# Kernel optimization log

Measured on AMD Instinct MI355X. Metric: run time of the kernel, lower is better.

Reference implementation:

```python
import jax, jax.numpy as jnp
import numpy as np

B, DIM, HEADS, H, W = 4, 64, 64, 256, 256


def _conv1x1(x, w):
    # x: [b,c,h,w], w: [o,c] -> [b,o,h,w]
    return jnp.einsum('bchw,oc->bohw', x, w)


def _conv3x3_s2_reflect(x, w, groups):
    # reflect pad 1, 3x3 conv, stride 2 (matches padding_mode='reflect', stride=2)
    xp = jnp.pad(x, ((0, 0), (0, 0), (1, 1), (1, 1)), mode='reflect')
    return jax.lax.conv_general_dilated(
        xp, w, window_strides=(2, 2), padding='VALID',
        dimension_numbers=('NCHW', 'OIHW', 'NCHW'), feature_group_count=groups)


def _to_heads(t, heads):
    # safe_rearrange: zero-pad channels to a multiple of heads, then b (head c) h w -> b head c (h w)
    b, c, h, w = t.shape
    if c % heads != 0:
        t = jnp.pad(t, ((0, 0), (0, heads - c % heads), (0, 0), (0, 0)))
        c = t.shape[1]
    return t.reshape(b, heads, c // heads, h * w)


def _l2norm(t, eps=1e-12):
    # F.normalize(dim=-1): x / max(||x||, eps)
    n = jnp.sqrt(jnp.sum(t * t, axis=-1, keepdims=True))
    return t / jnp.maximum(n, eps)


def setup_inputs() -> dict:
    key = jax.random.key(0)
    ks = jax.random.split(key, 13)
    d = DIM
    s = 0.05
    return {
        'x': jax.random.normal(ks[0], (B, d, H, W), jnp.float32),
        'illu_feat': jax.random.uniform(ks[1], (B, d, H, W), jnp.float32),
        'w_q_spec': jax.random.normal(ks[2], (d, d), jnp.float32) * s,
        'w_k_spec': jax.random.normal(ks[3], (d, d), jnp.float32) * s,
        'w_v_spec': jax.random.normal(ks[4], (d, d), jnp.float32) * s,
        'w_q_spat': jax.random.normal(ks[5], (d, 1, 3, 3), jnp.float32) * s,  # depthwise
        'w_k_spat': jax.random.normal(ks[6], (d, d, 3, 3), jnp.float32) * s,
        'w_v_spat': jax.random.normal(ks[7], (d, d), jnp.float32) * s,
        'w_anchor_dw': jax.random.normal(ks[8], (d, 1, 3, 3), jnp.float32) * s,  # depthwise
        'w_anchor_pw': jax.random.normal(ks[9], (d // 2, d), jnp.float32) * s,
        'w_proj': jax.random.normal(ks[10], (d, d), jnp.float32) * s,
        'temp_spec': jnp.ones((HEADS, 1, 1), jnp.float32),
        'temp_spat': jnp.ones((HEADS, 1, 1), jnp.float32),
    }


def reference(x, illu_feat, w_q_spec, w_k_spec, w_v_spec, w_q_spat, w_k_spat,
              w_v_spat, w_anchor_dw, w_anchor_pw, w_proj, temp_spec, temp_spat):
    b, c, h, w = x.shape
    heads = HEADS

    q_spec = _conv1x1(x, w_q_spec)
    k_spec = _conv1x1(x, w_k_spec)                       # computed but unused downstream (as in original)
    v_spec = _conv1x1(x, w_v_spec) * illu_feat
    q_spat = _conv3x3_s2_reflect(x, w_q_spat, groups=c)  # computed but unused downstream (as in original)
    k_spat = _conv3x3_s2_reflect(x, w_k_spat, groups=1)
    v_spat = _conv1x1(x, w_v_spat) * illu_feat
    anchor = _conv1x1(_conv3x3_s2_reflect(x, w_anchor_dw, groups=c), w_anchor_pw)

    q_spec = _l2norm(_to_heads(q_spec, heads))
    k_spec = _l2norm(_to_heads(k_spec, heads))
    v_spec = _to_heads(v_spec, heads)
    q_spat = _l2norm(_to_heads(q_spat, heads))
    k_spat = _to_heads(k_spat, heads)
    v_spat = _to_heads(v_spat, heads)
    anchor = _l2norm(_to_heads(anchor, heads))

    n_q = q_spec.shape[-1]      # h*w
    n_a = anchor.shape[-1]      # (h//2)*(w//2)
    n_v = v_spec.shape[-1]
    n_k = k_spat.shape[-1]

    # spectral branch: q x anchor (truncate to common spatial length)
    m = min(n_q, n_a)
    attn_spec = jnp.einsum('bhcn,bhdn->bhcd', q_spec[..., :m], anchor[..., :m]) * temp_spec
    attn_spec = jax.nn.softmax(attn_spec, axis=-1)

    # v_spec spatial matching via adaptive avg pool (static no-op here since n_v == n_q)
    if n_v != n_q:
        vh = int(n_v ** 0.5)
        qh = int(n_q ** 0.5)
        v4 = v_spec.reshape(b, heads, v_spec.shape[2], vh, vh)
        v4 = jax.image.resize(v4, (b, heads, v_spec.shape[2], qh, qh), method='linear')
        v_spec_matched = v4.reshape(b, heads, v_spec.shape[2], -1)
    else:
        v_spec_matched = v_spec

    # spatial branch: anchor x k_spat (truncate to common spatial length)
    m2 = min(n_a, n_k)
    attn_spat = jnp.einsum('bhcn,bhdn->bhcd', anchor[..., :m2], k_spat[..., :m2]) * temp_spat
    attn_spat = jax.nn.softmax(attn_spat, axis=-1)

    out_spec = jnp.einsum('bhcd,bhdn->bhcn', attn_spec, v_spec_matched)
    out_spat = jnp.einsum('bhcd,bhdn->bhcn', attn_spat, v_spat)

    m3 = min(out_spec.shape[-1], out_spat.shape[-1])
    out = 0.6 * out_spec[..., :m3] + 0.4 * out_spat[..., :m3]

    ah = int(m3 ** 0.5)
    out = out.reshape(b, heads * out.shape[2], ah, ah)
    if ah != h or ah != w:
        # F.interpolate bilinear, align_corners=False == half-pixel linear resize
        out = jax.image.resize(out, (b, out.shape[1], h, w), method='bilinear')
    out = out[:, :DIM]
    return _conv1x1(out, w_proj)
```

## Files before the change

### kernel.cpp

```cpp
#include <hip/hip_runtime.h>


#define HW 65536
#define CH 64
#define PT 64
#define SX 68

typedef short s4_t __attribute__((ext_vector_type(4)));
typedef short s8_t __attribute__((ext_vector_type(8)));
typedef float f4_t __attribute__((ext_vector_type(4)));

typedef const __attribute__((address_space(1))) unsigned int* gp_t;
typedef __attribute__((address_space(3))) unsigned int* lp_t;

static __device__ __forceinline__ unsigned short f2bf(float f) {
  unsigned u = __float_as_uint(f);
  return (unsigned short)((u + 0x7fffu + ((u >> 16) & 1u)) >> 16);
}
static __device__ __forceinline__ s8_t ld8(const unsigned short* p) {
  s4_t lo = *(const s4_t*)p;
  s4_t hi = *(const s4_t*)(p + 4);
  s8_t r = {lo[0], lo[1], lo[2], lo[3], hi[0], hi[1], hi[2], hi[3]};
  return r;
}
static __device__ __forceinline__ void gload16(const float* g, float* l) {
  __builtin_amdgcn_global_load_lds((gp_t)(unsigned long long)g,
                                   (lp_t)(unsigned long long)l, 16, 0, 0);
}

__global__ __launch_bounds__(256, 2) void fused_hsattn(
    const float* __restrict__ x, const float* __restrict__ illu,
    const float* __restrict__ wvs, const float* __restrict__ wvt,
    const float* __restrict__ wproj, float* __restrict__ out) {
  __shared__ __align__(16) float xs[CH * PT];
  __shared__ __align__(16) float ils[CH * PT];
  __shared__ __align__(16) unsigned short XH[PT * SX];
  __shared__ __align__(16) unsigned short WM[CH * SX];
  __shared__ __align__(16) unsigned short WP[CH * SX];

  const int tid  = threadIdx.x;
  const int bb   = blockIdx.x >> 10;
  const int pix0 = (blockIdx.x & 1023) << 6;
  const int base = bb * CH * HW + pix0;
  const int lane = tid & 63;
  const int wv   = tid >> 6;

  f4_t wa[4], wb[4], wc[4];
#pragma unroll
  for (int it = 0; it < 4; ++it) {
    int j4 = (it * 256 + tid) * 4;
    wa[it] = *(const f4_t*)(wvs + j4);
    wb[it] = *(const f4_t*)(wvt + j4);
    wc[it] = *(const f4_t*)(wproj + j4);
  }

#pragma unroll
  for (int it = 0; it < 4; ++it) {
    int u = wv * 1024 + it * 256;
    int f = u + lane * 4;
    int c = f >> 6, p = f & 63;
    gload16(x + base + c * HW + p, xs + u);
    gload16(illu + base + c * HW + p, ils + u);
  }

#pragma unroll
  for (int it = 0; it < 4; ++it) {
    int idx = it * 256 + tid;
    int r = idx >> 4, c4 = (idx & 15) * 4;
    s4_t m, w;
#pragma unroll
    for (int j = 0; j < 4; ++j) {
      m[j] = (short)f2bf(0.6f * wa[it][j] + 0.4f * wb[it][j]);
      w[j] = (short)f2bf(wc[it][j]);
    }
    *(s4_t*)(WM + r * SX + c4) = m;
    *(s4_t*)(WP + r * SX + c4) = w;
  }
  __syncthreads();

  {
    const int p = tid & 63, cc = (tid >> 6) << 4;
#pragma unroll
    for (int k = 0; k < 16; k += 2) {
      float f0 = xs[(cc + k) * PT + p];
      float f1 = xs[(cc + k + 1) * PT + p];
      unsigned pk = (unsigned)f2bf(f0) | ((unsigned)f2bf(f1) << 16);
      *(unsigned*)(XH + p * SX + cc + k) = pk;
    }
  }
  __syncthreads();

  const int n15 = lane & 15, q = lane >> 4;
  const int nb  = wv * 16;

  f4_t acc[4];
#pragma unroll
  for (int i = 0; i < 4; ++i) acc[i] = (f4_t){0.f, 0.f, 0.f, 0.f};
#pragma unroll
  for (int kc = 0; kc < 2; ++kc) {
    s8_t B = ld8(XH + (nb + n15) * SX + kc * 32 + q * 8);
#pragma unroll
    for (int mt = 0; mt < 4; ++mt) {
      s8_t A = ld8(WM + (mt * 16 + n15) * SX + kc * 32 + q * 8);
      acc[mt] = __builtin_amdgcn_mfma_f32_16x16x32_bf16(A, B, acc[mt], 0, 0, 0);
    }
  }

  s4_t uh[4];
#pragma unroll
  for (int mt = 0; mt < 4; ++mt) {
    s4_t h;
#pragma unroll
    for (int r = 0; r < 4; ++r) {
      int c = mt * 16 + q * 4 + r;
      h[r] = (short)f2bf(acc[mt][r] * ils[c * PT + nb + n15]);
    }
    uh[mt] = h;
  }
#pragma unroll
  for (int mt = 0; mt < 4; ++mt)
    *(s4_t*)(XH + (nb + n15) * SX + mt * 16 + q * 4) = uh[mt];

  f4_t acc2[4];
#pragma unroll
  for (int i = 0; i < 4; ++i) acc2[i] = (f4_t){0.f, 0.f, 0.f, 0.f};
#pragma unroll
  for (int kc = 0; kc < 2; ++kc) {
    s8_t B = ld8(XH + (nb + n15) * SX + kc * 32 + q * 8);
#pragma unroll
    for (int mt = 0; mt < 4; ++mt) {
      s8_t A = ld8(WP + (mt * 16 + n15) * SX + kc * 32 + q * 8);
      acc2[mt] = __builtin_amdgcn_mfma_f32_16x16x32_bf16(A, B, acc2[mt], 0, 0, 0);
    }
  }

#pragma unroll
  for (int mt = 0; mt < 4; ++mt) {
    float* op = out + base + (mt * 16 + q * 4) * HW + nb + n15;
    f4_t a = acc2[mt];
#pragma unroll
    for (int r = 0; r < 4; ++r) op[r * HW] = a[r];
  }
}

extern "C" void kernel_launch(void* const* d_in, const int* in_sizes, int n_in,
                              void* d_out, int out_size, void* d_ws, size_t ws_size,
                              hipStream_t stream) {
  const float* x     = (const float*)d_in[0];
  const float* illu  = (const float*)d_in[1];
  const float* wvs   = (const float*)d_in[4];
  const float* wvt   = (const float*)d_in[7];
  const float* wproj = (const float*)d_in[10];
  float* out = (float*)d_out;

  fused_hsattn<<<4 * (HW / PT), 256, 0, stream>>>(x, illu, wvs, wvt, wproj, out);
}
```

Measured before the change: 201.8 us.

## Load activations directly into MFMA registers and loop four tiles per block with prefetch

The kernel stops staging x and illu through LDS with global_load_lds. Each lane now loads its MFMA operand elements straight from global memory into registers. Each block processes four pixel tiles in sequence, prefetching the next tile's x and illu while computing the current one. This also spreads the per-block weight setup over more work and raises occupancy to 4 blocks per SM. In exchange the global loads become scalar and strided per lane, 4 bytes per channel row with 16 consecutive pixels, instead of 16-byte vector loads. Register pressure also rises, and there is no barrier between the XH write and read across tiles, which is only safe because each wave owns its own XH rows.

```diff
diff --git a/kernel.cpp b/kernel.cpp
--- a/kernel.cpp
+++ b/kernel.cpp
@@ -5,13 +5,11 @@
 #define CH 64
 #define PT 64
 #define SX 68
+#define TPB 4
 
 typedef short s4_t __attribute__((ext_vector_type(4)));
 typedef short s8_t __attribute__((ext_vector_type(8)));
 typedef float f4_t __attribute__((ext_vector_type(4)));
-
-typedef const __attribute__((address_space(1))) unsigned int* gp_t;
-typedef __attribute__((address_space(3))) unsigned int* lp_t;
 
 static __device__ __forceinline__ unsigned short f2bf(float f) {
   unsigned u = __float_as_uint(f);
@@ -23,27 +21,26 @@
   s8_t r = {lo[0], lo[1], lo[2], lo[3], hi[0], hi[1], hi[2], hi[3]};
   return r;
 }
-static __device__ __forceinline__ void gload16(const float* g, float* l) {
-  __builtin_amdgcn_global_load_lds((gp_t)(unsigned long long)g,
-                                   (lp_t)(unsigned long long)l, 16, 0, 0);
-}
 
-__global__ __launch_bounds__(256, 2) void fused_hsattn(
+__global__ __launch_bounds__(256, 4) void fused_hsattn(
     const float* __restrict__ x, const float* __restrict__ illu,
     const float* __restrict__ wvs, const float* __restrict__ wvt,
     const float* __restrict__ wproj, float* __restrict__ out) {
-  __shared__ __align__(16) float xs[CH * PT];
-  __shared__ __align__(16) float ils[CH * PT];
-  __shared__ __align__(16) unsigned short XH[PT * SX];
   __shared__ __align__(16) unsigned short WM[CH * SX];
   __shared__ __align__(16) unsigned short WP[CH * SX];
+  __shared__ __align__(16) unsigned short XH[PT * SX];
 
   const int tid  = threadIdx.x;
-  const int bb   = blockIdx.x >> 10;
-  const int pix0 = (blockIdx.x & 1023) << 6;
-  const int base = bb * CH * HW + pix0;
   const int lane = tid & 63;
   const int wv   = tid >> 6;
+  const int n15  = lane & 15;
+  const int q    = lane >> 4;
+  const int nb   = wv * 16;
+
+  const int tile0 = blockIdx.x * TPB;
+  const int bb    = tile0 >> 10;
+  const int pix0  = (tile0 & 1023) << 6;
+  const int base0 = bb * CH * HW + pix0;
 
   f4_t wa[4], wb[4], wc[4];
 #pragma unroll
@@ -54,13 +51,20 @@
     wc[it] = *(const f4_t*)(wproj + j4);
   }
 
+  float xv[16], iv[16];
+  {
+    const float* xb = x + base0 + nb + n15;
+    const float* ib = illu + base0 + nb + n15;
 #pragma unroll
-  for (int it = 0; it < 4; ++it) {
-    int u = wv * 1024 + it * 256;
-    int f = u + lane * 4;
-    int c = f >> 6, p = f & 63;
-    gload16(x + base + c * HW + p, xs + u);
-    gload16(illu + base + c * HW + p, ils + u);
+    for (int kc = 0; kc < 2; ++kc)
+#pragma unroll
+      for (int j = 0; j < 8; ++j)
+        xv[kc * 8 + j] = xb[(kc * 32 + q * 8 + j) * HW];
+#pragma unroll
+    for (int mt = 0; mt < 4; ++mt)
+#pragma unroll
+      for (int r = 0; r < 4; ++r)
+        iv[mt * 4 + r] = ib[(mt * 16 + q * 4 + r) * HW];
   }
 
 #pragma unroll
@@ -78,68 +82,75 @@
   }
   __syncthreads();
 
-  {
-    const int p = tid & 63, cc = (tid >> 6) << 4;
 #pragma unroll
-    for (int k = 0; k < 16; k += 2) {
-      float f0 = xs[(cc + k) * PT + p];
-      float f1 = xs[(cc + k + 1) * PT + p];
-      unsigned pk = (unsigned)f2bf(f0) | ((unsigned)f2bf(f1) << 16);
-      *(unsigned*)(XH + p * SX + cc + k) = pk;
+  for (int t = 0; t < TPB; ++t) {
+    const int base = base0 + t * PT;
+
+    s8_t B0, B1;
+#pragma unroll
+    for (int j = 0; j < 8; ++j) {
+      B0[j] = (short)f2bf(xv[j]);
+      B1[j] = (short)f2bf(xv[8 + j]);
     }
-  }
-  __syncthreads();
 
-  const int n15 = lane & 15, q = lane >> 4;
-  const int nb  = wv * 16;
+    if (t + 1 < TPB) {
+      const float* xb = x + base0 + (t + 1) * PT + nb + n15;
+#pragma unroll
+      for (int kc = 0; kc < 2; ++kc)
+#pragma unroll
+        for (int j = 0; j < 8; ++j)
+          xv[kc * 8 + j] = xb[(kc * 32 + q * 8 + j) * HW];
+    }
 
-  f4_t acc[4];
+    f4_t acc[4];
 #pragma unroll
-  for (int i = 0; i < 4; ++i) acc[i] = (f4_t){0.f, 0.f, 0.f, 0.f};
-#pragma unroll
-  for (int kc = 0; kc < 2; ++kc) {
-    s8_t B = ld8(XH + (nb + n15) * SX + kc * 32 + q * 8);
+    for (int i = 0; i < 4; ++i) acc[i] = (f4_t){0.f, 0.f, 0.f, 0.f};
 #pragma unroll
     for (int mt = 0; mt < 4; ++mt) {
-      s8_t A = ld8(WM + (mt * 16 + n15) * SX + kc * 32 + q * 8);
-      acc[mt] = __builtin_amdgcn_mfma_f32_16x16x32_bf16(A, B, acc[mt], 0, 0, 0);
+      s8_t A0 = ld8(WM + (mt * 16 + n15) * SX + q * 8);
+      acc[mt] = __builtin_amdgcn_mfma_f32_16x16x32_bf16(A0, B0, acc[mt], 0, 0, 0);
+      s8_t A1 = ld8(WM + (mt * 16 + n15) * SX + 32 + q * 8);
+      acc[mt] = __builtin_amdgcn_mfma_f32_16x16x32_bf16(A1, B1, acc[mt], 0, 0, 0);
     }
-  }
 
-  s4_t uh[4];
-#pragma unroll
-  for (int mt = 0; mt < 4; ++mt) {
-    s4_t h;
-#pragma unroll
-    for (int r = 0; r < 4; ++r) {
-      int c = mt * 16 + q * 4 + r;
-      h[r] = (short)f2bf(acc[mt][r] * ils[c * PT + nb + n15]);
-    }
-    uh[mt] = h;
-  }
-#pragma unroll
-  for (int mt = 0; mt < 4; ++mt)
-    *(s4_t*)(XH + (nb + n15) * SX + mt * 16 + q * 4) = uh[mt];
-
-  f4_t acc2[4];
-#pragma unroll
-  for (int i = 0; i < 4; ++i) acc2[i] = (f4_t){0.f, 0.f, 0.f, 0.f};
-#pragma unroll
-  for (int kc = 0; kc < 2; ++kc) {
-    s8_t B = ld8(XH + (nb + n15) * SX + kc * 32 + q * 8);
 #pragma unroll
     for (int mt = 0; mt < 4; ++mt) {
-      s8_t A = ld8(WP + (mt * 16 + n15) * SX + kc * 32 + q * 8);
-      acc2[mt] = __builtin_amdgcn_mfma_f32_16x16x32_bf16(A, B, acc2[mt], 0, 0, 0);
+      s4_t h;
+#pragma unroll
+      for (int r = 0; r < 4; ++r)
+        h[r] = (short)f2bf(acc[mt][r] * iv[mt * 4 + r]);
+      *(s4_t*)(XH + (nb + n15) * SX + mt * 16 + q * 4) = h;
     }
-  }
+
+    if (t + 1 < TPB) {
+      const float* ib = illu + base0 + (t + 1) * PT + nb + n15;
+#pragma unroll
+      for (int mt = 0; mt < 4; ++mt)
+#pragma unroll
+        for (int r = 0; r < 4; ++r)
+          iv[mt * 4 + r] = ib[(mt * 16 + q * 4 + r) * HW];
+    }
+
+    f4_t acc2[4];
+#pragma unroll
+    for (int i = 0; i < 4; ++i) acc2[i] = (f4_t){0.f, 0.f, 0.f, 0.f};
+#pragma unroll
+    for (int kc = 0; kc < 2; ++kc) {
+      s8_t B = ld8(XH + (nb + n15) * SX + kc * 32 + q * 8);
+#pragma unroll
+      for (int mt = 0; mt < 4; ++mt) {
+        s8_t A = ld8(WP + (mt * 16 + n15) * SX + kc * 32 + q * 8);
+        acc2[mt] = __builtin_amdgcn_mfma_f32_16x16x32_bf16(A, B, acc2[mt], 0, 0, 0);
+      }
+    }
 
 #pragma unroll
-  for (int mt = 0; mt < 4; ++mt) {
-    float* op = out + base + (mt * 16 + q * 4) * HW + nb + n15;
-    f4_t a = acc2[mt];
+    for (int mt = 0; mt < 4; ++mt) {
+      float* op = out + base + (mt * 16 + q * 4) * HW + nb + n15;
+      f4_t a = acc2[mt];
 #pragma unroll
-    for (int r = 0; r < 4; ++r) op[r * HW] = a[r];
+      for (int r = 0; r < 4; ++r) op[r * HW] = a[r];
+    }
   }
 }
 
@@ -153,5 +164,6 @@
   const float* wproj = (const float*)d_in[10];
   float* out = (float*)d_out;
 
-  fused_hsattn<<<4 * (HW / PT), 256, 0, stream>>>(x, illu, wvs, wvt, wproj, out);
+  fused_hsattn<<<4 * (HW / PT) / TPB, 256, 0, stream>>>(x, illu, wvs, wvt,
+                                                        wproj, out);
 }
```

After: 274.9 us. +36.3%, slower.

## Process multiple 128-pixel tiles per block with register-prefetched loads

Applied to the files above, without the earlier changes.

Each block now handles four tiles of 128 pixels instead of one 64-pixel tile. Inputs are loaded into registers and the next tile is prefetched while the current one is computed. The async global-to-LDS path and the fp32 x staging buffer are gone: x goes straight from registers into LDS as transposed bf16, and illu is stored with a padded stride. The goal is to cut the per-block cost of weight setup and launch and to overlap memory latency with MFMA work, at the cost of more registers and fewer blocks.

```diff
diff --git a/kernel.cpp b/kernel.cpp
--- a/kernel.cpp
+++ b/kernel.cpp
@@ -1,17 +1,16 @@
 #include <hip/hip_runtime.h>
 
 
-#define HW 65536
-#define CH 64
-#define PT 64
-#define SX 68
+#define HW    65536
+#define CHHW  (64 * 65536)
+#define PT    128
+#define SXT   68
+#define SIL   132
+#define TPB   4
 
 typedef short s4_t __attribute__((ext_vector_type(4)));
 typedef short s8_t __attribute__((ext_vector_type(8)));
 typedef float f4_t __attribute__((ext_vector_type(4)));
-
-typedef const __attribute__((address_space(1))) unsigned int* gp_t;
-typedef __attribute__((address_space(3))) unsigned int* lp_t;
 
 static __device__ __forceinline__ unsigned short f2bf(float f) {
   unsigned u = __float_as_uint(f);
@@ -23,27 +22,24 @@
   s8_t r = {lo[0], lo[1], lo[2], lo[3], hi[0], hi[1], hi[2], hi[3]};
   return r;
 }
-static __device__ __forceinline__ void gload16(const float* g, float* l) {
-  __builtin_amdgcn_global_load_lds((gp_t)(unsigned long long)g,
-                                   (lp_t)(unsigned long long)l, 16, 0, 0);
-}
 
 __global__ __launch_bounds__(256, 2) void fused_hsattn(
     const float* __restrict__ x, const float* __restrict__ illu,
     const float* __restrict__ wvs, const float* __restrict__ wvt,
     const float* __restrict__ wproj, float* __restrict__ out) {
-  __shared__ __align__(16) float xs[CH * PT];
-  __shared__ __align__(16) float ils[CH * PT];
-  __shared__ __align__(16) unsigned short XH[PT * SX];
-  __shared__ __align__(16) unsigned short WM[CH * SX];
-  __shared__ __align__(16) unsigned short WP[CH * SX];
+  __shared__ __align__(16) unsigned short WM[64 * SXT];
+  __shared__ __align__(16) unsigned short WP[64 * SXT];
+  __shared__ __align__(16) unsigned short XT[PT * SXT];
+  __shared__ __align__(16) float ILS[64 * SIL];
 
   const int tid  = threadIdx.x;
-  const int bb   = blockIdx.x >> 10;
-  const int pix0 = (blockIdx.x & 1023) << 6;
-  const int base = bb * CH * HW + pix0;
   const int lane = tid & 63;
   const int wv   = tid >> 6;
+  const int n15  = lane & 15;
+  const int q    = lane >> 4;
+
+  const int ch0 = wv * 16 + (lane >> 5);
+  const int pxl = (lane & 31) * 4;
 
   f4_t wa[4], wb[4], wc[4];
 #pragma unroll
@@ -54,13 +50,16 @@
     wc[it] = *(const f4_t*)(wproj + j4);
   }
 
+  f4_t xr[8], ir[8];
+  {
+    const int g    = blockIdx.x * TPB;
+    const int base = (g >> 9) * CHHW + ((g & 511) << 7);
 #pragma unroll
-  for (int it = 0; it < 4; ++it) {
-    int u = wv * 1024 + it * 256;
-    int f = u + lane * 4;
-    int c = f >> 6, p = f & 63;
-    gload16(x + base + c * HW + p, xs + u);
-    gload16(illu + base + c * HW + p, ils + u);
+    for (int it = 0; it < 8; ++it) {
+      const int off = base + (ch0 + 2 * it) * HW + pxl;
+      xr[it] = *(const f4_t*)(x + off);
+      ir[it] = *(const f4_t*)(illu + off);
+    }
   }
 
 #pragma unroll
@@ -73,73 +72,88 @@
       m[j] = (short)f2bf(0.6f * wa[it][j] + 0.4f * wb[it][j]);
       w[j] = (short)f2bf(wc[it][j]);
     }
-    *(s4_t*)(WM + r * SX + c4) = m;
-    *(s4_t*)(WP + r * SX + c4) = w;
-  }
-  __syncthreads();
-
-  {
-    const int p = tid & 63, cc = (tid >> 6) << 4;
-#pragma unroll
-    for (int k = 0; k < 16; k += 2) {
-      float f0 = xs[(cc + k) * PT + p];
-      float f1 = xs[(cc + k + 1) * PT + p];
-      unsigned pk = (unsigned)f2bf(f0) | ((unsigned)f2bf(f1) << 16);
-      *(unsigned*)(XH + p * SX + cc + k) = pk;
-    }
-  }
-  __syncthreads();
-
-  const int n15 = lane & 15, q = lane >> 4;
-  const int nb  = wv * 16;
-
-  f4_t acc[4];
-#pragma unroll
-  for (int i = 0; i < 4; ++i) acc[i] = (f4_t){0.f, 0.f, 0.f, 0.f};
-#pragma unroll
-  for (int kc = 0; kc < 2; ++kc) {
-    s8_t B = ld8(XH + (nb + n15) * SX + kc * 32 + q * 8);
-#pragma unroll
-    for (int mt = 0; mt < 4; ++mt) {
-      s8_t A = ld8(WM + (mt * 16 + n15) * SX + kc * 32 + q * 8);
-      acc[mt] = __builtin_amdgcn_mfma_f32_16x16x32_bf16(A, B, acc[mt], 0, 0, 0);
-    }
-  }
-
-  s4_t uh[4];
-#pragma unroll
-  for (int mt = 0; mt < 4; ++mt) {
-    s4_t h;
-#pragma unroll
-    for (int r = 0; r < 4; ++r) {
-      int c = mt * 16 + q * 4 + r;
-      h[r] = (short)f2bf(acc[mt][r] * ils[c * PT + nb + n15]);
-    }
-    uh[mt] = h;
-  }
-#pragma unroll
-  for (int mt = 0; mt < 4; ++mt)
-    *(s4_t*)(XH + (nb + n15) * SX + mt * 16 + q * 4) = uh[mt];
-
-  f4_t acc2[4];
-#pragma unroll
-  for (int i = 0; i < 4; ++i) acc2[i] = (f4_t){0.f, 0.f, 0.f, 0.f};
-#pragma unroll
-  for (int kc = 0; kc < 2; ++kc) {
-    s8_t B = ld8(XH + (nb + n15) * SX + kc * 32 + q * 8);
-#pragma unroll
-    for (int mt = 0; mt < 4; ++mt) {
-      s8_t A = ld8(WP + (mt * 16 + n15) * SX + kc * 32 + q * 8);
-      acc2[mt] = __builtin_amdgcn_mfma_f32_16x16x32_bf16(A, B, acc2[mt], 0, 0, 0);
-    }
+    *(s4_t*)(WM + r * SXT + c4) = m;
+    *(s4_t*)(WP + r * SXT + c4) = w;
   }
 
 #pragma unroll
-  for (int mt = 0; mt < 4; ++mt) {
-    float* op = out + base + (mt * 16 + q * 4) * HW + nb + n15;
-    f4_t a = acc2[mt];
+  for (int t = 0; t < TPB; ++t) {
+    const int g    = blockIdx.x * TPB + t;
+    const int base = (g >> 9) * CHHW + ((g & 511) << 7);
+
 #pragma unroll
-    for (int r = 0; r < 4; ++r) op[r * HW] = a[r];
+    for (int it = 0; it < 8; ++it) {
+      const int ch = ch0 + 2 * it;
+      f4_t v = xr[it];
+#pragma unroll
+      for (int j = 0; j < 4; ++j)
+        XT[(pxl + j) * SXT + ch] = f2bf(v[j]);
+      *(f4_t*)(ILS + ch * SIL + pxl) = ir[it];
+    }
+    __syncthreads();
+
+    if (t + 1 < TPB) {
+      const int g2 = g + 1;
+      const int b2 = (g2 >> 9) * CHHW + ((g2 & 511) << 7);
+#pragma unroll
+      for (int it = 0; it < 8; ++it) {
+        const int off = b2 + (ch0 + 2 * it) * HW + pxl;
+        xr[it] = *(const f4_t*)(x + off);
+        ir[it] = *(const f4_t*)(illu + off);
+      }
+    }
+
+#pragma unroll
+    for (int nt = 0; nt < 2; ++nt) {
+      const int pr = wv * 32 + nt * 16;
+      unsigned short* xrow = XT + (pr + n15) * SXT;
+
+      f4_t acc[4];
+#pragma unroll
+      for (int i = 0; i < 4; ++i) acc[i] = (f4_t){0.f, 0.f, 0.f, 0.f};
+#pragma unroll
+      for (int kc = 0; kc < 2; ++kc) {
+        s8_t B = ld8(xrow + kc * 32 + q * 8);
+#pragma unroll
+        for (int mt = 0; mt < 4; ++mt) {
+          s8_t A = ld8(WM + (mt * 16 + n15) * SXT + kc * 32 + q * 8);
+          acc[mt] = __builtin_amdgcn_mfma_f32_16x16x32_bf16(A, B, acc[mt], 0, 0, 0);
+        }
+      }
+
+#pragma unroll
+      for (int mt = 0; mt < 4; ++mt) {
+        s4_t h;
+#pragma unroll
+        for (int r = 0; r < 4; ++r) {
+          const int c = mt * 16 + q * 4 + r;
+          h[r] = (short)f2bf(acc[mt][r] * ILS[c * SIL + pr + n15]);
+        }
+        *(s4_t*)(xrow + mt * 16 + q * 4) = h;
+      }
+
+      f4_t acc2[4];
+#pragma unroll
+      for (int i = 0; i < 4; ++i) acc2[i] = (f4_t){0.f, 0.f, 0.f, 0.f};
+#pragma unroll
+      for (int kc = 0; kc < 2; ++kc) {
+        s8_t B = ld8(xrow + kc * 32 + q * 8);
+#pragma unroll
+        for (int mt = 0; mt < 4; ++mt) {
+          s8_t A = ld8(WP + (mt * 16 + n15) * SXT + kc * 32 + q * 8);
+          acc2[mt] = __builtin_amdgcn_mfma_f32_16x16x32_bf16(A, B, acc2[mt], 0, 0, 0);
+        }
+      }
+
+#pragma unroll
+      for (int mt = 0; mt < 4; ++mt) {
+        float* op = out + base + (mt * 16 + q * 4) * HW + pr + n15;
+        f4_t a = acc2[mt];
+#pragma unroll
+        for (int r = 0; r < 4; ++r) op[r * HW] = a[r];
+      }
+    }
+    __syncthreads();
   }
 }
 
@@ -153,5 +167,6 @@
   const float* wproj = (const float*)d_in[10];
   float* out = (float*)d_out;
 
-  fused_hsattn<<<4 * (HW / PT), 256, 0, stream>>>(x, illu, wvs, wvt, wproj, out);
+  fused_hsattn<<<(4 * (HW / PT)) / TPB, 256, 0, stream>>>(x, illu, wvs, wvt,
+                                                          wproj, out);
 }
```

Measured after the change: 203.3 us. No clear change (+0.8%).
